# Optimization experiments

Hardware: AMD Instinct MI355X
Metric: run time of the kernel (lower is better)

The kernel has to match this reference:

```python
import jax, jax.numpy as jnp
import numpy as np

D_MODEL = 1024
N_HEADS = 16
D_HEAD = D_MODEL // N_HEADS
B, T = 4, 2048


def setup_inputs() -> dict:
    key = jax.random.key(0)
    ks = jax.random.split(key, 7)
    s = 0.02
    q = jax.random.normal(ks[0], (B, T, D_MODEL), dtype=jnp.float32)
    k = jax.random.normal(ks[1], (B, T, D_MODEL), dtype=jnp.float32)
    v = jax.random.normal(ks[2], (B, T, D_MODEL), dtype=jnp.float32)
    # causal mask, True = masked (strict upper triangle)
    mask = jnp.triu(jnp.ones((T, T), dtype=bool), k=1)[None, None, :, :]
    Wq = jax.random.normal(ks[3], (D_MODEL, D_MODEL), dtype=jnp.float32) * s
    Wk = jax.random.normal(ks[4], (D_MODEL, D_MODEL), dtype=jnp.float32) * s
    Wv = jax.random.normal(ks[5], (D_MODEL, D_MODEL), dtype=jnp.float32) * s
    Wo = jax.random.normal(ks[6], (D_MODEL, D_MODEL), dtype=jnp.float32) * s
    return {"q": q, "k": k, "v": v, "mask": mask,
            "Wq": Wq, "Wk": Wk, "Wv": Wv, "Wo": Wo}


def reference(q, k, v, mask, Wq, Wk, Wv, Wo):
    H, Dh = N_HEADS, D_HEAD
    scale = Dh ** -0.5

    def split(t):  # [B,T,D] -> [B,H,T,Dh]
        Bt, Tt, _ = t.shape
        return t.reshape(Bt, Tt, H, Dh).transpose(0, 2, 1, 3)

    # torch Linear (no bias): y = x @ W.T
    Q = split(q @ Wq.T)
    K = split(k @ Wk.T)
    V = split(v @ Wv.T)

    scores = jnp.einsum('bhqd,bhkd->bhqk', Q, K) * scale
    scores = jnp.where(mask, -jnp.inf, scores)
    attn = jax.nn.softmax(scores, axis=-1)
    attn = jnp.nan_to_num(attn)  # fully-masked rows -> 0
    out = jnp.einsum('bhqk,bhkd->bhqd', attn, V)
    out = out.transpose(0, 2, 1, 3).reshape(q.shape[0], q.shape[1], H * Dh)
    return out @ Wo.T
```

## Files before the change

### kernel.cpp

```cpp
#include <hip/hip_runtime.h>
#include <stdint.h>

#define D_MODEL 1024
#define N_HEADS 16
#define D_HEAD 64
#define BATCH 4
#define SEQ 2048
#define MTOT (BATCH * SEQ)

typedef unsigned short u16;
typedef __attribute__((ext_vector_type(8))) short bf16x8;
typedef __attribute__((ext_vector_type(4))) float f32x4;

#define MFMA(a, b, c) __builtin_amdgcn_mfma_f32_16x16x32_bf16((a), (b), (c), 0, 0, 0)

static __device__ __forceinline__ u16 f2bf(float f) {
  unsigned u = __builtin_bit_cast(unsigned, f);
  u += 0x7fffu + ((u >> 16) & 1u);
  return (u16)(u >> 16);
}
static __device__ __forceinline__ u16 f2bf_t(float f) {
  return (u16)(__builtin_bit_cast(unsigned, f) >> 16);
}

static __device__ __forceinline__ void gload_lds16(const void* g, void* l) {
  __builtin_amdgcn_global_load_lds(
      (const __attribute__((address_space(1))) void*)g,
      (__attribute__((address_space(3))) void*)l, 16, 0, 0);
}

__global__ __launch_bounds__(256) void cvt3(const float* __restrict__ a,
                                            const float* __restrict__ b,
                                            const float* __restrict__ c,
                                            u16* __restrict__ oa, u16* __restrict__ ob,
                                            u16* __restrict__ oc) {
  const int z = blockIdx.y;
  const float* in = (z == 0) ? a : (z == 1) ? b : c;
  u16* out = (z == 0) ? oa : (z == 1) ? ob : oc;
  int i = blockIdx.x * 256 + threadIdx.x;
  float4 v = ((const float4*)in)[i];
  ushort4 o;
  o.x = f2bf(v.x); o.y = f2bf(v.y); o.z = f2bf(v.z); o.w = f2bf(v.w);
  ((ushort4*)out)[i] = o;
}

__global__ __launch_bounds__(256) void cvt4(const float* __restrict__ a,
                                            const float* __restrict__ b,
                                            const float* __restrict__ c,
                                            const float* __restrict__ d,
                                            u16* __restrict__ oa, u16* __restrict__ ob,
                                            u16* __restrict__ oc, u16* __restrict__ od) {
  const int z = blockIdx.y;
  const float* in = (z == 0) ? a : (z == 1) ? b : (z == 2) ? c : d;
  u16* out = (z == 0) ? oa : (z == 1) ? ob : (z == 2) ? oc : od;
  int i = blockIdx.x * 256 + threadIdx.x;
  float4 v = ((const float4*)in)[i];
  ushort4 o;
  o.x = f2bf(v.x); o.y = f2bf(v.y); o.z = f2bf(v.z); o.w = f2bf(v.w);
  ((ushort4*)out)[i] = o;
}


__global__ __launch_bounds__(256) void gemm_qkv(const u16* __restrict__ xq,
                                                const u16* __restrict__ xk,
                                                const u16* __restrict__ xv,
                                                const u16* __restrict__ Wqb,
                                                const u16* __restrict__ Wkb,
                                                const u16* __restrict__ Wvb,
                                                u16* __restrict__ Qb, u16* __restrict__ Kb,
                                                u16* __restrict__ Vtg, int zbase) {
  __shared__ u16 As[128 * 64];
  __shared__ u16 Bs[128 * 64];
  const int z = blockIdx.z + zbase;
  const u16* A = (z == 0) ? xq : (z == 1) ? xk : xv;
  const u16* B = (z == 0) ? Wqb : (z == 1) ? Wkb : Wvb;

  const int t = threadIdx.x;
  const int lane = t & 63, wave = t >> 6;
  const int wm = wave & 1, wn = wave >> 1;
  const int lrow = lane & 15, quad = lane >> 4;
  const int m0 = blockIdx.x * 128, n0 = blockIdx.y * 128;
  const int srow = t >> 3;
  const int swcol = (((t & 7) ^ (srow & 7)) << 3);
  const int rsw = lrow & 7;

  f32x4 acc[4][4];
#pragma unroll
  for (int i = 0; i < 4; i++)
#pragma unroll
    for (int j = 0; j < 4; j++) acc[i][j] = (f32x4){0.f, 0.f, 0.f, 0.f};

  for (int k0 = 0; k0 < 1024; k0 += 64) {
#pragma unroll
    for (int r = 0; r < 4; ++r) {
      int rr = r * 32 + srow;
      gload_lds16(A + (size_t)(m0 + rr) * 1024 + k0 + swcol, As + rr * 64 + (t & 7) * 8);
      gload_lds16(B + (size_t)(n0 + rr) * 1024 + k0 + swcol, Bs + rr * 64 + (t & 7) * 8);
    }
    __syncthreads();
#pragma unroll
    for (int ks = 0; ks < 2; ++ks) {
      const int cx = ((ks * 4 + quad) ^ rsw) << 3;
      bf16x8 a[4], b[4];
#pragma unroll
      for (int i = 0; i < 4; i++)
        a[i] = *(const bf16x8*)(As + (wm * 64 + i * 16 + lrow) * 64 + cx);
#pragma unroll
      for (int j = 0; j < 4; j++)
        b[j] = *(const bf16x8*)(Bs + (wn * 64 + j * 16 + lrow) * 64 + cx);
#pragma unroll
      for (int i = 0; i < 4; i++)
#pragma unroll
        for (int j = 0; j < 4; j++) acc[i][j] = MFMA(a[i], b[j], acc[i][j]);
    }
    __syncthreads();
  }
  if (z == 2) {
    const int b = m0 >> 11;
    const int t0 = (m0 & 2047);
#pragma unroll
    for (int i = 0; i < 4; i++) {
      const int trow = t0 + wm * 64 + i * 16 + quad * 4;
#pragma unroll
      for (int j = 0; j < 4; j++) {
        const int n = n0 + wn * 64 + j * 16 + lrow;
        ushort4 pk;
        pk.x = f2bf(acc[i][j][0]); pk.y = f2bf(acc[i][j][1]);
        pk.z = f2bf(acc[i][j][2]); pk.w = f2bf(acc[i][j][3]);
        *(ushort4*)(Vtg + (size_t)b * D_MODEL * SEQ + (size_t)n * SEQ + trow) = pk;
      }
    }
  } else {
    u16* C = z ? Kb : Qb;
#pragma unroll
    for (int i = 0; i < 4; i++) {
      const int mr = m0 + wm * 64 + i * 16 + quad * 4;
#pragma unroll
      for (int j = 0; j < 4; j++) {
        const int n = n0 + wn * 64 + j * 16 + lrow;
#pragma unroll
        for (int r = 0; r < 4; r++) C[(size_t)(mr + r) * 1024 + n] = f2bf(acc[i][j][r]);
      }
    }
  }
}

__global__ __launch_bounds__(256) void gemm_o(const u16* __restrict__ A,
                                              const u16* __restrict__ B,
                                              float* __restrict__ C) {
  __shared__ u16 As[128 * 64];
  __shared__ u16 Bs[128 * 64];
  const int t = threadIdx.x;
  const int lane = t & 63, wave = t >> 6;
  const int wm = wave & 1, wn = wave >> 1;
  const int lrow = lane & 15, quad = lane >> 4;
  const int m0 = blockIdx.x * 128, n0 = blockIdx.y * 128;
  const int srow = t >> 3;
  const int swcol = (((t & 7) ^ (srow & 7)) << 3);
  const int rsw = lrow & 7;

  f32x4 acc[4][4];
#pragma unroll
  for (int i = 0; i < 4; i++)
#pragma unroll
    for (int j = 0; j < 4; j++) acc[i][j] = (f32x4){0.f, 0.f, 0.f, 0.f};

  for (int k0 = 0; k0 < 1024; k0 += 64) {
#pragma unroll
    for (int r = 0; r < 4; ++r) {
      int rr = r * 32 + srow;
      gload_lds16(A + (size_t)(m0 + rr) * 1024 + k0 + swcol, As + rr * 64 + (t & 7) * 8);
      gload_lds16(B + (size_t)(n0 + rr) * 1024 + k0 + swcol, Bs + rr * 64 + (t & 7) * 8);
    }
    __syncthreads();
#pragma unroll
    for (int ks = 0; ks < 2; ++ks) {
      const int cx = ((ks * 4 + quad) ^ rsw) << 3;
      bf16x8 a[4], b[4];
#pragma unroll
      for (int i = 0; i < 4; i++)
        a[i] = *(const bf16x8*)(As + (wm * 64 + i * 16 + lrow) * 64 + cx);
#pragma unroll
      for (int j = 0; j < 4; j++)
        b[j] = *(const bf16x8*)(Bs + (wn * 64 + j * 16 + lrow) * 64 + cx);
#pragma unroll
      for (int i = 0; i < 4; i++)
#pragma unroll
        for (int j = 0; j < 4; j++) acc[i][j] = MFMA(a[i], b[j], acc[i][j]);
    }
    __syncthreads();
  }
#pragma unroll
  for (int i = 0; i < 4; i++) {
    const int mr = m0 + wm * 64 + i * 16 + quad * 4;
#pragma unroll
    for (int j = 0; j < 4; j++) {
      const int n = n0 + wn * 64 + j * 16 + lrow;
#pragma unroll
      for (int r = 0; r < 4; r++) C[(size_t)(mr + r) * 1024 + n] = acc[i][j][r];
    }
  }
}

#define LOG2E 1.4426950408889634f
#define SC (0.125f * LOG2E)

__global__ __launch_bounds__(256) void attn_causal(const u16* __restrict__ Qb,
                                                   const u16* __restrict__ Kb,
                                                   const u16* __restrict__ Vtg,
                                                   u16* __restrict__ Ob) {
  __shared__ u16 Qs[64 * 64];
  __shared__ u16 Ks[64 * 64];
  __shared__ u16 Vs[64 * 64];
  __shared__ u16 Ps[64 * 64];

  const int t = threadIdx.x;
  const int lane = t & 63, wave = t >> 6;
  const int lrow = lane & 15, quad = lane >> 4;
  const int bh = blockIdx.y;
  const int b = bh >> 4, h = bh & 15;
  const int col0 = h * 64;
  const size_t rowbase = (size_t)b * SEQ;
  const size_t vbase = (size_t)b * D_MODEL * SEQ;
  const int srow = t >> 3;
  const int swcol = (((t & 7) ^ (srow & 7)) << 3);
  const int pchunk = (t & 7) * 8;
  const int rsw = lrow & 7;

  bf16x8 aOnes;
  {
    const short ov = (lrow == 0) ? (short)0x3F80 : (short)0;
#pragma unroll
    for (int e = 0; e < 8; ++e) aOnes[e] = ov;
  }

  for (int part = 0; part < 2; ++part) {
    const int qt = part ? (31 - (int)blockIdx.x) : (int)blockIdx.x;
    const int qrow0 = qt * 64;

#pragma unroll
    for (int r = 0; r < 2; ++r) {
      int rr = r * 32 + srow;
      gload_lds16(Qb + (rowbase + qrow0 + rr) * D_MODEL + col0 + swcol,
                  Qs + rr * 64 + pchunk);
    }

    f32x4 oacc[4];
    f32x4 lacc;
#pragma unroll
    for (int d = 0; d < 4; d++) oacc[d] = (f32x4){0.f, 0.f, 0.f, 0.f};
    lacc = (f32x4){0.f, 0.f, 0.f, 0.f};

    const int nkt = qt + 1;
    for (int kt = 0; kt < nkt; ++kt) {
      const int j0 = kt * 64;
      __syncthreads();
#pragma unroll
      for (int r = 0; r < 2; ++r) {
        int rr = r * 32 + srow;
        gload_lds16(Kb + (rowbase + j0 + rr) * D_MODEL + col0 + swcol,
                    Ks + rr * 64 + pchunk);
        gload_lds16(Vtg + vbase + (size_t)(col0 + rr) * SEQ + j0 + swcol,
                    Vs + rr * 64 + pchunk);
      }
      __syncthreads();

      f32x4 sacc[4];
#pragma unroll
      for (int j = 0; j < 4; j++) sacc[j] = (f32x4){0.f, 0.f, 0.f, 0.f};
#pragma unroll
      for (int ks = 0; ks < 2; ++ks) {
        const int cx = ((ks * 4 + quad) ^ rsw) << 3;
        bf16x8 aq = *(const bf16x8*)(Qs + (wave * 16 + lrow) * 64 + cx);
#pragma unroll
        for (int jc = 0; jc < 4; jc++) {
          bf16x8 bk = *(const bf16x8*)(Ks + (jc * 16 + lrow) * 64 + cx);
          sacc[jc] = MFMA(aq, bk, sacc[jc]);
        }
      }

      const bool diag = (kt == qt);
#pragma unroll
      for (int r = 0; r < 4; r++) {
        const int mrow = wave * 16 + quad * 4 + r;
        const int grow = qrow0 + mrow;
#pragma unroll
        for (int jc = 0; jc < 4; jc++) {
          float p = __builtin_amdgcn_exp2f(sacc[jc][r] * SC);
          if (diag && (j0 + jc * 16 + lrow > grow)) p = 0.f;
          const int cc = ((jc * 2 + (lrow >> 3)) ^ (mrow & 7)) << 3;
          Ps[(mrow << 6) + cc + (lrow & 7)] = f2bf_t(p);
        }
      }

#pragma unroll
      for (int ks = 0; ks < 2; ++ks) {
        const int cx = ((ks * 4 + quad) ^ rsw) << 3;
        bf16x8 bP = *(const bf16x8*)(Ps + ((wave * 16 + lrow) << 6) + cx);
        lacc = MFMA(aOnes, bP, lacc);
#pragma unroll
        for (int d = 0; d < 4; d++) {
          bf16x8 aV = *(const bf16x8*)(Vs + (d * 16 + lrow) * 64 + cx);
          oacc[d] = MFMA(aV, bP, oacc[d]);
        }
      }
    }
    __syncthreads();

    const float linv = 1.0f / __shfl(lacc[0], lrow);

    u16* orow = Ob + (rowbase + qrow0 + wave * 16 + lrow) * D_MODEL + col0;
#pragma unroll
    for (int d = 0; d < 4; d++) {
      f32x4 o = oacc[d];
      ushort4 pk;
      pk.x = f2bf(o[0] * linv); pk.y = f2bf(o[1] * linv);
      pk.z = f2bf(o[2] * linv); pk.w = f2bf(o[3] * linv);
      *(ushort4*)(orow + d * 16 + quad * 4) = pk;
    }
  }
}

extern "C" void kernel_launch(void* const* d_in, const int* in_sizes, int n_in,
                              void* d_out, int out_size, void* d_ws, size_t ws_size,
                              hipStream_t stream) {
  const float* q  = (const float*)d_in[0];
  const float* k  = (const float*)d_in[1];
  const float* v  = (const float*)d_in[2];
  const float* Wq = (const float*)d_in[4];
  const float* Wk = (const float*)d_in[5];
  const float* Wv = (const float*)d_in[6];
  const float* Wo = (const float*)d_in[7];
  float* out = (float*)d_out;

  char* ws = (char*)d_ws;
  const size_t MB = 1 << 20;
  u16* xq  = (u16*)(ws);
  u16* xk  = (u16*)(ws + 16 * MB);
  u16* xv  = (u16*)(ws + 32 * MB);
  u16* Wqb = (u16*)(ws + 48 * MB);
  u16* Wkb = (u16*)(ws + 50 * MB);
  u16* Wvb = (u16*)(ws + 52 * MB);
  u16* Wob = (u16*)(ws + 54 * MB);
  u16* Qb  = (u16*)(ws + 56 * MB);

  const dim3 cb(256);
  cvt3<<<dim3(MTOT * D_MODEL / 4 / 256, 3), cb, 0, stream>>>(q, k, v, xq, xk, xv);
  cvt4<<<dim3(D_MODEL * D_MODEL / 4 / 256, 4), cb, 0, stream>>>(Wq, Wk, Wv, Wo,
                                                                Wqb, Wkb, Wvb, Wob);

  if (ws_size >= 104 * MB) {
    u16* Kb  = (u16*)(ws + 72 * MB);
    u16* Vtg = (u16*)(ws + 88 * MB);
    gemm_qkv<<<dim3(64, 8, 3), cb, 0, stream>>>(xq, xk, xv, Wqb, Wkb, Wvb,
                                                Qb, Kb, Vtg, 0);
    attn_causal<<<dim3(16, 64), cb, 0, stream>>>(Qb, Kb, Vtg, xq);
    gemm_o<<<dim3(64, 8), cb, 0, stream>>>(xq, Wob, out);
  } else {
    u16* Kb  = (u16*)(ws);
    u16* Vtg = (u16*)(ws + 16 * MB);
    u16* Oatt = (u16*)(ws + 32 * MB);
    gemm_qkv<<<dim3(64, 8, 1), cb, 0, stream>>>(xq, xq, xq, Wqb, Wqb, Wqb,
                                                Qb, Qb, Qb, 0);
    gemm_qkv<<<dim3(64, 8, 1), cb, 0, stream>>>(xk, xk, xk, Wkb, Wkb, Wkb,
                                                Kb, Kb, Kb, 1);
    gemm_qkv<<<dim3(64, 8, 1), cb, 0, stream>>>(xv, xv, xv, Wvb, Wvb, Wvb,
                                                Vtg, Vtg, Vtg, 2);
    attn_causal<<<dim3(16, 64), cb, 0, stream>>>(Qb, Kb, Vtg, Oatt);
    gemm_o<<<dim3(64, 8), cb, 0, stream>>>(Oatt, Wob, out);
  }
}
```

Before: 355.2 us.

## Enlarge attention query tile to 128 rows and fold softmax scale into Wq

```diff
diff --git a/kernel.cpp b/kernel.cpp
--- a/kernel.cpp
+++ b/kernel.cpp
@@ -13,6 +13,8 @@
 typedef __attribute__((ext_vector_type(4))) float f32x4;
 
 #define MFMA(a, b, c) __builtin_amdgcn_mfma_f32_16x16x32_bf16((a), (b), (c), 0, 0, 0)
+#define LOG2E 1.4426950408889634f
+#define SC (0.125f * LOG2E)
 
 static __device__ __forceinline__ u16 f2bf(float f) {
   unsigned u = __builtin_bit_cast(unsigned, f);
@@ -53,10 +55,11 @@
   const int z = blockIdx.y;
   const float* in = (z == 0) ? a : (z == 1) ? b : (z == 2) ? c : d;
   u16* out = (z == 0) ? oa : (z == 1) ? ob : (z == 2) ? oc : od;
+  const float s = (z == 0) ? SC : 1.0f;
   int i = blockIdx.x * 256 + threadIdx.x;
   float4 v = ((const float4*)in)[i];
   ushort4 o;
-  o.x = f2bf(v.x); o.y = f2bf(v.y); o.z = f2bf(v.z); o.w = f2bf(v.w);
+  o.x = f2bf(v.x * s); o.y = f2bf(v.y * s); o.z = f2bf(v.z * s); o.w = f2bf(v.w * s);
   ((ushort4*)out)[i] = o;
 }
 
@@ -202,56 +205,57 @@
   }
 }
 
-#define LOG2E 1.4426950408889634f
-#define SC (0.125f * LOG2E)
-
 __global__ __launch_bounds__(256) void attn_causal(const u16* __restrict__ Qb,
                                                    const u16* __restrict__ Kb,
                                                    const u16* __restrict__ Vtg,
                                                    u16* __restrict__ Ob) {
-  __shared__ u16 Qs[64 * 64];
+  __shared__ u16 QPs[128 * 64];
   __shared__ u16 Ks[64 * 64];
   __shared__ u16 Vs[64 * 64];
-  __shared__ u16 Ps[64 * 64];
 
   const int t = threadIdx.x;
   const int lane = t & 63, wave = t >> 6;
   const int lrow = lane & 15, quad = lane >> 4;
-  const int bh = blockIdx.y;
+  const int wb = wave * 32;
+  const int bh = blockIdx.x;
   const int b = bh >> 4, h = bh & 15;
   const int col0 = h * 64;
   const size_t rowbase = (size_t)b * SEQ;
-  const size_t vbase = (size_t)b * D_MODEL * SEQ;
+  const size_t vbase = (size_t)b * (size_t)D_MODEL * SEQ;
   const int srow = t >> 3;
   const int swcol = (((t & 7) ^ (srow & 7)) << 3);
   const int pchunk = (t & 7) * 8;
   const int rsw = lrow & 7;
 
-  bf16x8 aOnes;
+  bf16x8 bOnes;
   {
     const short ov = (lrow == 0) ? (short)0x3F80 : (short)0;
 #pragma unroll
-    for (int e = 0; e < 8; ++e) aOnes[e] = ov;
+    for (int e = 0; e < 8; ++e) bOnes[e] = ov;
   }
 
   for (int part = 0; part < 2; ++part) {
-    const int qt = part ? (31 - (int)blockIdx.x) : (int)blockIdx.x;
-    const int qrow0 = qt * 64;
-
-#pragma unroll
-    for (int r = 0; r < 2; ++r) {
+    const int qt = part ? (15 - (int)blockIdx.y) : (int)blockIdx.y;
+    const int qrow0 = qt * 128;
+
+#pragma unroll
+    for (int r = 0; r < 4; ++r) {
       int rr = r * 32 + srow;
       gload_lds16(Qb + (rowbase + qrow0 + rr) * D_MODEL + col0 + swcol,
-                  Qs + rr * 64 + pchunk);
-    }
-
-    f32x4 oacc[4];
-    f32x4 lacc;
-#pragma unroll
-    for (int d = 0; d < 4; d++) oacc[d] = (f32x4){0.f, 0.f, 0.f, 0.f};
-    lacc = (f32x4){0.f, 0.f, 0.f, 0.f};
-
-    const int nkt = qt + 1;
+                  QPs + rr * 64 + pchunk);
+    }
+
+    bf16x8 bQ[2][2];
+    f32x4 oacc[2][4];
+    f32x4 lacc[2];
+#pragma unroll
+    for (int mf = 0; mf < 2; mf++) {
+#pragma unroll
+      for (int df = 0; df < 4; df++) oacc[mf][df] = (f32x4){0.f, 0.f, 0.f, 0.f};
+      lacc[mf] = (f32x4){0.f, 0.f, 0.f, 0.f};
+    }
+
+    const int nkt = 2 * qt + 2;
     for (int kt = 0; kt < nkt; ++kt) {
       const int j0 = kt * 64;
       __syncthreads();
@@ -265,59 +269,82 @@
       }
       __syncthreads();
 
-      f32x4 sacc[4];
-#pragma unroll
-      for (int j = 0; j < 4; j++) sacc[j] = (f32x4){0.f, 0.f, 0.f, 0.f};
+      if (kt == 0) {
+#pragma unroll
+        for (int mf = 0; mf < 2; ++mf)
+#pragma unroll
+          for (int ks = 0; ks < 2; ++ks)
+            bQ[mf][ks] = *(const bf16x8*)(QPs + (wb + mf * 16 + lrow) * 64 +
+                                          (((ks * 4 + quad) ^ rsw) << 3));
+      }
+
+      const bool diag = (kt >= 2 * qt);
+#pragma unroll
+      for (int mf = 0; mf < 2; ++mf) {
+        f32x4 st[4];
+#pragma unroll
+        for (int jf = 0; jf < 4; jf++) st[jf] = (f32x4){0.f, 0.f, 0.f, 0.f};
+#pragma unroll
+        for (int ks = 0; ks < 2; ++ks) {
+          const int cx = ((ks * 4 + quad) ^ rsw) << 3;
+#pragma unroll
+          for (int jf = 0; jf < 4; jf++) {
+            bf16x8 aK = *(const bf16x8*)(Ks + (jf * 16 + lrow) * 64 + cx);
+            st[jf] = MFMA(aK, bQ[mf][ks], st[jf]);
+          }
+        }
+        const int m = wb + mf * 16 + lrow;
+        const int gm = qrow0 + m;
+#pragma unroll
+        for (int jf = 0; jf < 4; jf++) {
+          ushort4 pk;
+#pragma unroll
+          for (int r = 0; r < 4; r++) {
+            float p = __builtin_amdgcn_exp2f(st[jf][r]);
+            const int gj = j0 + jf * 16 + quad * 4 + r;
+            if (diag && gj > gm) p = 0.f;
+            ((u16*)&pk)[r] = f2bf_t(p);
+          }
+          const int j = jf * 16 + quad * 4;
+          *(ushort4*)(QPs + m * 64 + ((((j >> 3) ^ (m & 7)) << 3) | (j & 7))) = pk;
+        }
+      }
+
 #pragma unroll
       for (int ks = 0; ks < 2; ++ks) {
         const int cx = ((ks * 4 + quad) ^ rsw) << 3;
-        bf16x8 aq = *(const bf16x8*)(Qs + (wave * 16 + lrow) * 64 + cx);
-#pragma unroll
-        for (int jc = 0; jc < 4; jc++) {
-          bf16x8 bk = *(const bf16x8*)(Ks + (jc * 16 + lrow) * 64 + cx);
-          sacc[jc] = MFMA(aq, bk, sacc[jc]);
+        bf16x8 aP[2];
+#pragma unroll
+        for (int mf = 0; mf < 2; ++mf)
+          aP[mf] = *(const bf16x8*)(QPs + (wb + mf * 16 + lrow) * 64 + cx);
+        lacc[0] = MFMA(aP[0], bOnes, lacc[0]);
+        lacc[1] = MFMA(aP[1], bOnes, lacc[1]);
+#pragma unroll
+        for (int df = 0; df < 4; df++) {
+          bf16x8 bV = *(const bf16x8*)(Vs + (df * 16 + lrow) * 64 + cx);
+          oacc[0][df] = MFMA(aP[0], bV, oacc[0][df]);
+          oacc[1][df] = MFMA(aP[1], bV, oacc[1][df]);
         }
       }
-
-      const bool diag = (kt == qt);
+    }
+    __syncthreads();
+
+    float linv[2][4];
+#pragma unroll
+    for (int mf = 0; mf < 2; mf++)
+#pragma unroll
+      for (int r = 0; r < 4; r++)
+        linv[mf][r] = 1.0f / __shfl(lacc[mf][r], lane & 48);
+
+#pragma unroll
+    for (int mf = 0; mf < 2; mf++)
 #pragma unroll
       for (int r = 0; r < 4; r++) {
-        const int mrow = wave * 16 + quad * 4 + r;
-        const int grow = qrow0 + mrow;
-#pragma unroll
-        for (int jc = 0; jc < 4; jc++) {
-          float p = __builtin_amdgcn_exp2f(sacc[jc][r] * SC);
-          if (diag && (j0 + jc * 16 + lrow > grow)) p = 0.f;
-          const int cc = ((jc * 2 + (lrow >> 3)) ^ (mrow & 7)) << 3;
-          Ps[(mrow << 6) + cc + (lrow & 7)] = f2bf_t(p);
-        }
-      }
-
-#pragma unroll
-      for (int ks = 0; ks < 2; ++ks) {
-        const int cx = ((ks * 4 + quad) ^ rsw) << 3;
-        bf16x8 bP = *(const bf16x8*)(Ps + ((wave * 16 + lrow) << 6) + cx);
-        lacc = MFMA(aOnes, bP, lacc);
-#pragma unroll
-        for (int d = 0; d < 4; d++) {
-          bf16x8 aV = *(const bf16x8*)(Vs + (d * 16 + lrow) * 64 + cx);
-          oacc[d] = MFMA(aV, bP, oacc[d]);
-        }
-      }
-    }
-    __syncthreads();
-
-    const float linv = 1.0f / __shfl(lacc[0], lrow);
-
-    u16* orow = Ob + (rowbase + qrow0 + wave * 16 + lrow) * D_MODEL + col0;
-#pragma unroll
-    for (int d = 0; d < 4; d++) {
-      f32x4 o = oacc[d];
-      ushort4 pk;
-      pk.x = f2bf(o[0] * linv); pk.y = f2bf(o[1] * linv);
-      pk.z = f2bf(o[2] * linv); pk.w = f2bf(o[3] * linv);
-      *(ushort4*)(orow + d * 16 + quad * 4) = pk;
-    }
+        u16* orow = Ob + (rowbase + qrow0 + wb + mf * 16 + quad * 4 + r) * D_MODEL + col0;
+#pragma unroll
+        for (int df = 0; df < 4; df++)
+          orow[df * 16 + lrow] = f2bf(oacc[mf][df][r] * linv[mf][r]);
+      }
   }
 }
 
@@ -354,7 +381,7 @@
     u16* Vtg = (u16*)(ws + 88 * MB);
     gemm_qkv<<<dim3(64, 8, 3), cb, 0, stream>>>(xq, xk, xv, Wqb, Wkb, Wvb,
                                                 Qb, Kb, Vtg, 0);
-    attn_causal<<<dim3(16, 64), cb, 0, stream>>>(Qb, Kb, Vtg, xq);
+    attn_causal<<<dim3(64, 8), cb, 0, stream>>>(Qb, Kb, Vtg, xq);
     gemm_o<<<dim3(64, 8), cb, 0, stream>>>(xq, Wob, out);
   } else {
     u16* Kb  = (u16*)(ws);
@@ -366,7 +393,7 @@
                                                 Kb, Kb, Kb, 1);
     gemm_qkv<<<dim3(64, 8, 1), cb, 0, stream>>>(xv, xv, xv, Wvb, Wvb, Wvb,
                                                 Vtg, Vtg, Vtg, 2);
-    attn_causal<<<dim3(16, 64), cb, 0, stream>>>(Qb, Kb, Vtg, Oatt);
+    attn_causal<<<dim3(64, 8), cb, 0, stream>>>(Qb, Kb, Vtg, Oatt);
     gemm_o<<<dim3(64, 8), cb, 0, stream>>>(Oatt, Wob, out);
   }
 }
```

Result: faster. 313.8 us (-11.6%).
